# Kernel optimization log

Measured on AMD Instinct MI355X. Metric: run time of the kernel, lower is better.

The kernel has to match this reference:

```python
import jax, jax.numpy as jnp
import numpy as np

IN_DIM = 128
OUT_DIM = 64
ALPHA = 0.2  # LeakyReLU negative slope


def _xavier(key, shape):
    # matches nn.init.xavier_uniform_ with gain=1.414
    fan_in, fan_out = shape
    limit = 1.414 * np.sqrt(6.0 / (fan_in + fan_out))
    return jax.random.uniform(key, shape, jnp.float32, -limit, limit)


def setup_inputs() -> dict:
    key = jax.random.key(0)
    ks = jax.random.split(key, 12)
    N_C, N_P, N_I, E = 200000, 200000, 100000, 1000000
    return {
        "taxPayer_feats": jax.random.normal(ks[0], (N_C, IN_DIM), jnp.float32),
        "person_feats": jax.random.normal(ks[1], (N_P, IN_DIM), jnp.float32),
        "item_feats": jax.random.normal(ks[2], (N_I, IN_DIM), jnp.float32),
        "idx_c0": jax.random.randint(ks[3], (E,), 0, N_C, jnp.int64 if jax.config.jax_enable_x64 else jnp.int32),
        "idx_c1": jax.random.randint(ks[4], (E,), 0, N_C, jnp.int64 if jax.config.jax_enable_x64 else jnp.int32),
        "idx_p": jax.random.randint(ks[5], (E,), 0, N_P, jnp.int64 if jax.config.jax_enable_x64 else jnp.int32),
        "P_company": _xavier(ks[6], (IN_DIM, OUT_DIM)),
        "P_person": _xavier(ks[7], (IN_DIM, OUT_DIM)),
        "P_item": _xavier(ks[8], (IN_DIM, OUT_DIM)),
        "W_PCC": _xavier(ks[9], (OUT_DIM * 3, OUT_DIM)),
    }


def reference(taxPayer_feats, person_feats, item_feats, idx_c0, idx_c1, idx_p,
              P_company, P_person, P_item, W_PCC):
    # InstanceAggLayer.forward, pattern_name='PCC'
    f_taxPayer = taxPayer_feats @ P_company   # [N_C, D]
    f_person = person_feats @ P_person        # [N_P, D]
    f_item = item_feats @ P_item              # computed in original (unused for PCC)
    d = f_taxPayer.shape[1]
    # cat([f_c[i0], f_c[i1], f_p[i2]], dim=1) @ W_PCC  ==  sum of slice matmuls
    # (same math, avoids materializing the [E, 3D] concat)
    pre = (f_taxPayer[idx_c0] @ W_PCC[:d]
           + f_taxPayer[idx_c1] @ W_PCC[d:2 * d]
           + f_person[idx_p] @ W_PCC[2 * d:])
    instance = jnp.where(pre >= 0, pre, ALPHA * pre)  # LeakyReLU
    return instance
```

## Files before the change

kernel.cpp:

```cpp
#include <hip/hip_runtime.h>

#define IN_DIM 128
#define OUT_DIM 64
#define ALPHA 0.2f

typedef __attribute__((ext_vector_type(8))) short short8v;
typedef __attribute__((ext_vector_type(4))) float f32x4;
typedef __attribute__((ext_vector_type(4))) unsigned int u32x4;

__device__ __forceinline__ unsigned short bf16rne(float x) {
    union { float f; unsigned u; } c; c.f = x;
    const unsigned u = c.u;
    return (unsigned short)((u + 0x7fffu + ((u >> 16) & 1u)) >> 16);
}

__global__ __launch_bounds__(256) void compute_M_kernel(
    const float* __restrict__ P_company,
    const float* __restrict__ P_person,
    const float* __restrict__ W_PCC,
    float* __restrict__ M,
    unsigned short* __restrict__ Mt)
{
    const int mb = blockIdx.x >> 4;
    const int chunk = blockIdx.x & 15;
    const float* __restrict__ P = (mb == 2) ? P_person : P_company;
    const float* __restrict__ Wb = W_PCC + mb * OUT_DIM * OUT_DIM;
    float* __restrict__ Mb = M + mb * IN_DIM * OUT_DIM;
    const int base = chunk * 512;
    for (int idx = base + threadIdx.x; idx < base + 512; idx += 256) {
        const int r = idx >> 6;
        const int c = idx & 63;
        float acc = 0.f;
#pragma unroll
        for (int k = 0; k < OUT_DIM; ++k)
            acc = fmaf(P[r * OUT_DIM + k], Wb[k * OUT_DIM + c], acc);
        Mb[idx] = acc;
        Mt[(mb * OUT_DIM + c) * IN_DIM + r] = bf16rne(acc);
    }
}

union F4 { f32x4 v; float f[4]; };

__device__ __forceinline__ void load_A(F4* L, const float* __restrict__ feats,
                                       int nrows, int tile, int fr, int fq) {
    long long ar = (long long)tile * 16 + fr;
    if (ar >= nrows) ar = nrows - 1;
    const float* __restrict__ A = feats + ar * IN_DIM;
#pragma unroll
    for (int k0i = 0; k0i < 4; ++k0i) {
        L[k0i * 2 + 0].v = __builtin_nontemporal_load(
            (const f32x4*)(A + k0i * 32 + fq * 4));
        L[k0i * 2 + 1].v = __builtin_nontemporal_load(
            (const f32x4*)(A + k0i * 32 + 16 + fq * 4));
    }
}

__device__ __forceinline__ void table_body(
    const float* __restrict__ feats, int nrows,
    const unsigned short* __restrict__ Mtb,
    unsigned short* __restrict__ out,
    int tile0, int tstride)
{
    const int lane = threadIdx.x & 63;
    const int fr   = lane & 15;
    const int fq   = lane >> 4;

    union FragU { short8v v; uint2 q[2]; };
    short8v bfrag[4][4];
#pragma unroll
    for (int k0i = 0; k0i < 4; ++k0i)
#pragma unroll
        for (int c0i = 0; c0i < 4; ++c0i) {
            const unsigned short* p =
                Mtb + ((size_t)(c0i * 16 + fr)) * IN_DIM + k0i * 32 + fq * 4;
            FragU f;
            f.q[0] = *(const uint2*)(p);
            f.q[1] = *(const uint2*)(p + 16);
            bfrag[k0i][c0i] = f.v;
        }

    const int ntiles = (nrows + 15) >> 4;
    union AF { short8v v; unsigned short u[8]; };

    int tile = tile0;
    if (tile >= ntiles) return;
    F4 La[8];
    load_A(La, feats, nrows, tile, fr, fq);

    for (; tile < ntiles; tile += tstride) {
        const int next = tile + tstride;
        F4 Lb[8];
        if (next < ntiles) load_A(Lb, feats, nrows, next, fr, fq);

        short8v afrag[4];
#pragma unroll
        for (int k0i = 0; k0i < 4; ++k0i) {
            AF af;
#pragma unroll
            for (int j = 0; j < 4; ++j) {
                af.u[j]     = bf16rne(La[k0i * 2 + 0].f[j]);
                af.u[4 + j] = bf16rne(La[k0i * 2 + 1].f[j]);
            }
            afrag[k0i] = af.v;
        }

        f32x4 acc[4];
#pragma unroll
        for (int c0i = 0; c0i < 4; ++c0i) acc[c0i] = (f32x4){0.f, 0.f, 0.f, 0.f};
#pragma unroll
        for (int k0i = 0; k0i < 4; ++k0i)
#pragma unroll
            for (int c0i = 0; c0i < 4; ++c0i)
                acc[c0i] = __builtin_amdgcn_mfma_f32_16x16x32_bf16(
                    afrag[k0i], bfrag[k0i][c0i], acc[c0i], 0, 0, 0);

        const long long row0 = (long long)tile * 16;
#pragma unroll
        for (int c0i = 0; c0i < 4; ++c0i)
#pragma unroll
            for (int j = 0; j < 4; ++j) {
                const long long rg = row0 + fq * 4 + j;
                if (rg < nrows)
                    out[rg * OUT_DIM + c0i * 16 + fr] = bf16rne(acc[c0i][j]);
            }

#pragma unroll
        for (int i = 0; i < 8; ++i) La[i] = Lb[i];
    }
}

__global__ __launch_bounds__(256) void tables_kernel(
    const float* __restrict__ T, int n_c,
    const float* __restrict__ Pp, int n_p,
    const unsigned short* __restrict__ Mt,
    unsigned short* __restrict__ g0,
    unsigned short* __restrict__ g2,
    int gsplit)
{
    const int w = threadIdx.x >> 6;
    if ((int)blockIdx.x < gsplit) {
        const int table = w & 1;
        const int tile0 = (int)blockIdx.x * 2 + (w >> 1);
        table_body(T, n_c,
                   Mt + (size_t)table * OUT_DIM * IN_DIM,
                   g0 + (size_t)table * n_c * OUT_DIM,
                   tile0, gsplit * 2);
    } else {
        const int bid = (int)blockIdx.x - gsplit;
        const int nb  = (int)gridDim.x - gsplit;
        table_body(Pp, n_p,
                   Mt + (size_t)2 * OUT_DIM * IN_DIM,
                   g2, bid * 4 + w, nb * 4);
    }
}

__global__ __launch_bounds__(256) void gather_kernel(
    const int* __restrict__ i0, const int* __restrict__ i1, const int* __restrict__ i2,
    const unsigned short* __restrict__ g0, const unsigned short* __restrict__ g1,
    const unsigned short* __restrict__ g2,
    float* __restrict__ out, long long E)
{
    const long long t = (long long)blockIdx.x * 256 + threadIdx.x;
    const long long grp = t >> 3;
    const int j = (int)t & 7;
    const long long e0 = grp * 4;
    if (e0 >= E) return;

    long long e[4];
    bool live[4];
#pragma unroll
    for (int k = 0; k < 4; ++k) {
        e[k] = e0 + k;
        live[k] = e[k] < E;
        if (!live[k]) e[k] = E - 1;
    }

    int a0[4], a1[4], a2[4];
#pragma unroll
    for (int k = 0; k < 4; ++k) {
        a0[k] = __builtin_nontemporal_load(i0 + e[k]);
        a1[k] = __builtin_nontemporal_load(i1 + e[k]);
        a2[k] = __builtin_nontemporal_load(i2 + e[k]);
    }

    u32x4 v0[4], v1[4], v2[4];
#pragma unroll
    for (int k = 0; k < 4; ++k) {
        v0[k] = *(const u32x4*)(g0 + (long long)a0[k] * OUT_DIM + j * 8);
        v1[k] = *(const u32x4*)(g1 + (long long)a1[k] * OUT_DIM + j * 8);
        v2[k] = *(const u32x4*)(g2 + (long long)a2[k] * OUT_DIM + j * 8);
    }

#pragma unroll
    for (int k = 0; k < 4; ++k) {
        float s[8];
#pragma unroll
        for (int m = 0; m < 4; ++m) {
            const unsigned u0 = v0[k][m], u1 = v1[k][m], u2 = v2[k][m];
            const float lo = __uint_as_float(u0 << 16)
                           + __uint_as_float(u1 << 16)
                           + __uint_as_float(u2 << 16);
            const float hi = __uint_as_float(u0 & 0xffff0000u)
                           + __uint_as_float(u1 & 0xffff0000u)
                           + __uint_as_float(u2 & 0xffff0000u);
            s[2 * m]     = lo >= 0.f ? lo : ALPHA * lo;
            s[2 * m + 1] = hi >= 0.f ? hi : ALPHA * hi;
        }
        if (live[k]) {
            float* __restrict__ o = out + e[k] * OUT_DIM + j * 8;
            const f32x4 q0 = {s[0], s[1], s[2], s[3]};
            const f32x4 q1 = {s[4], s[5], s[6], s[7]};
            __builtin_nontemporal_store(q0, (f32x4*)(o));
            __builtin_nontemporal_store(q1, (f32x4*)(o + 4));
        }
    }
}

__global__ __launch_bounds__(256) void fused_fallback_kernel(
    const float* __restrict__ T, const float* __restrict__ Pp,
    const int* __restrict__ i0, const int* __restrict__ i1, const int* __restrict__ i2,
    const float* __restrict__ M, float* __restrict__ out, long long E)
{
    const int wave = threadIdx.x >> 6;
    const int lane = threadIdx.x & 63;
    const long long wavesTotal = (long long)gridDim.x * 4;
    const float* __restrict__ M0 = M;
    const float* __restrict__ M1 = M + IN_DIM * OUT_DIM;
    const float* __restrict__ M2 = M + 2 * IN_DIM * OUT_DIM;
    for (long long e = (long long)blockIdx.x * 4 + wave; e < E; e += wavesTotal) {
        const float* __restrict__ x0 = T + (long long)i0[e] * IN_DIM;
        const float* __restrict__ x1 = T + (long long)i1[e] * IN_DIM;
        const float* __restrict__ x2 = Pp + (long long)i2[e] * IN_DIM;
        float acc = 0.f;
#pragma unroll 4
        for (int k = 0; k < IN_DIM; ++k) {
            acc = fmaf(x0[k], M0[k * OUT_DIM + lane], acc);
            acc = fmaf(x1[k], M1[k * OUT_DIM + lane], acc);
            acc = fmaf(x2[k], M2[k * OUT_DIM + lane], acc);
        }
        acc = acc >= 0.f ? acc : ALPHA * acc;
        out[e * OUT_DIM + lane] = acc;
    }
}

extern "C" void kernel_launch(void* const* d_in, const int* in_sizes, int n_in,
                              void* d_out, int out_size, void* d_ws, size_t ws_size,
                              hipStream_t stream) {
    const float* T    = (const float*)d_in[0];
    const float* Pp   = (const float*)d_in[1];
    const int*   i0   = (const int*)d_in[3];
    const int*   i1   = (const int*)d_in[4];
    const int*   i2   = (const int*)d_in[5];
    const float* Pc   = (const float*)d_in[6];
    const float* Pper = (const float*)d_in[7];
    const float* W    = (const float*)d_in[9];
    float* out = (float*)d_out;

    const int n_c = in_sizes[0] / IN_DIM;
    const int n_p = in_sizes[1] / IN_DIM;
    const long long E = in_sizes[3];

    float* M = (float*)d_ws;
    unsigned short* Mt = (unsigned short*)((char*)d_ws + 98304);
    const size_t tblOff = 98304 + 49152;
    const size_t tblBytes = ((size_t)n_c * 2 + (size_t)n_p) * OUT_DIM * sizeof(unsigned short);

    compute_M_kernel<<<48, 256, 0, stream>>>(Pc, Pper, W, M, Mt);

    if (ws_size >= tblOff + tblBytes) {
        unsigned short* g0 = (unsigned short*)((char*)d_ws + tblOff);
        unsigned short* g1 = g0 + (size_t)n_c * OUT_DIM;
        unsigned short* g2 = g1 + (size_t)n_c * OUT_DIM;

        const int GA = 1024;
        const int GB = 512;
        tables_kernel<<<GA + GB, 256, 0, stream>>>(T, n_c, Pp, n_p, Mt, g0, g2, GA);

        const long long groups = (E + 3) / 4;
        const long long threads = groups * 8;
        gather_kernel<<<(int)((threads + 255) / 256), 256, 0, stream>>>(
            i0, i1, i2, g0, g1, g2, out, E);
    } else {
        fused_fallback_kernel<<<16384, 256, 0, stream>>>(T, Pp, i0, i1, i2, M, out, E);
    }
}
```

Baseline: 203.8 us.

## Stage feature rows in LDS as bf16 and use one block per tile

The tables kernel now gives each block a 64-row tile. The block loads that tile cooperatively with coalesced float4 reads, converts it to bf16 once, and stores it in shared memory. For the company table, both projection waves then read the same staged rows, so each feature row is converted once instead of once per table. The old persistent grid-stride loop with register prefetch is replaced by a grid sized to the row count, which removes manual software pipelining in exchange for more blocks and a barrier. The gather kernel also switches from nontemporal to ordinary index loads and output stores.

```diff
diff --git a/kernel.cpp b/kernel.cpp
--- a/kernel.cpp
+++ b/kernel.cpp
@@ -3,6 +3,8 @@
 #define IN_DIM 128
 #define OUT_DIM 64
 #define ALPHA 0.2f
+#define TROWS 64
+#define LROW (IN_DIM + 4)
 
 typedef __attribute__((ext_vector_type(8))) short short8v;
 typedef __attribute__((ext_vector_type(4))) float f32x4;
@@ -39,31 +41,39 @@
     }
 }
 
-union F4 { f32x4 v; float f[4]; };
-
-__device__ __forceinline__ void load_A(F4* L, const float* __restrict__ feats,
-                                       int nrows, int tile, int fr, int fq) {
-    long long ar = (long long)tile * 16 + fr;
-    if (ar >= nrows) ar = nrows - 1;
-    const float* __restrict__ A = feats + ar * IN_DIM;
-#pragma unroll
-    for (int k0i = 0; k0i < 4; ++k0i) {
-        L[k0i * 2 + 0].v = __builtin_nontemporal_load(
-            (const f32x4*)(A + k0i * 32 + fq * 4));
-        L[k0i * 2 + 1].v = __builtin_nontemporal_load(
-            (const f32x4*)(A + k0i * 32 + 16 + fq * 4));
-    }
-}
-
-__device__ __forceinline__ void table_body(
-    const float* __restrict__ feats, int nrows,
-    const unsigned short* __restrict__ Mtb,
-    unsigned short* __restrict__ out,
-    int tile0, int tstride)
-{
+__global__ __launch_bounds__(256) void tables_kernel(
+    const float* __restrict__ T, int n_c,
+    const float* __restrict__ Pp, int n_p,
+    const unsigned short* __restrict__ Mt,
+    unsigned short* __restrict__ g0,
+    unsigned short* __restrict__ g2,
+    int gsplit)
+{
+    __shared__ unsigned short xs[TROWS][LROW];
+    const int w    = threadIdx.x >> 6;
     const int lane = threadIdx.x & 63;
     const int fr   = lane & 15;
     const int fq   = lane >> 4;
+
+    const float* __restrict__ feats;
+    const unsigned short* __restrict__ Mtb;
+    unsigned short* __restrict__ outp;
+    int nrows, t0, tcount;
+    long long row0;
+    if ((int)blockIdx.x < gsplit) {
+        feats = T; nrows = n_c;
+        row0  = (long long)blockIdx.x * TROWS;
+        const int table = w & 1;
+        Mtb  = Mt + (size_t)table * OUT_DIM * IN_DIM;
+        outp = g0 + (size_t)table * n_c * OUT_DIM;
+        t0 = (w >> 1) * 2; tcount = 2;
+    } else {
+        feats = Pp; nrows = n_p;
+        row0  = (long long)((int)blockIdx.x - gsplit) * TROWS;
+        Mtb  = Mt + (size_t)2 * OUT_DIM * IN_DIM;
+        outp = g2;
+        t0 = w; tcount = 1;
+    }
 
     union FragU { short8v v; uint2 q[2]; };
     short8v bfrag[4][4];
@@ -79,28 +89,28 @@
             bfrag[k0i][c0i] = f.v;
         }
 
-    const int ntiles = (nrows + 15) >> 4;
-    union AF { short8v v; unsigned short u[8]; };
-
-    int tile = tile0;
-    if (tile >= ntiles) return;
-    F4 La[8];
-    load_A(La, feats, nrows, tile, fr, fq);
-
-    for (; tile < ntiles; tile += tstride) {
-        const int next = tile + tstride;
-        F4 Lb[8];
-        if (next < ntiles) load_A(Lb, feats, nrows, next, fr, fq);
-
+    for (int i = threadIdx.x; i < TROWS * (IN_DIM / 4); i += 256) {
+        const int r  = i >> 5;
+        const int c4 = i & 31;
+        long long gr = row0 + r;
+        if (gr >= nrows) gr = nrows - 1;
+        const float4 v = *(const float4*)(feats + gr * IN_DIM + c4 * 4);
+        union { unsigned short s[4]; uint2 q; } b;
+        b.s[0] = bf16rne(v.x); b.s[1] = bf16rne(v.y);
+        b.s[2] = bf16rne(v.z); b.s[3] = bf16rne(v.w);
+        *(uint2*)&xs[r][c4 * 4] = b.q;
+    }
+    __syncthreads();
+
+    const bool full = (row0 + TROWS) <= (long long)nrows;
+    for (int ti = 0; ti < tcount; ++ti) {
+        const int t = t0 + ti;
         short8v afrag[4];
 #pragma unroll
         for (int k0i = 0; k0i < 4; ++k0i) {
-            AF af;
-#pragma unroll
-            for (int j = 0; j < 4; ++j) {
-                af.u[j]     = bf16rne(La[k0i * 2 + 0].f[j]);
-                af.u[4 + j] = bf16rne(La[k0i * 2 + 1].f[j]);
-            }
+            FragU af;
+            af.q[0] = *(const uint2*)&xs[t * 16 + fr][k0i * 32 + fq * 4];
+            af.q[1] = *(const uint2*)&xs[t * 16 + fr][k0i * 32 + 16 + fq * 4];
             afrag[k0i] = af.v;
         }
 
@@ -114,43 +124,24 @@
                 acc[c0i] = __builtin_amdgcn_mfma_f32_16x16x32_bf16(
                     afrag[k0i], bfrag[k0i][c0i], acc[c0i], 0, 0, 0);
 
-        const long long row0 = (long long)tile * 16;
-#pragma unroll
-        for (int c0i = 0; c0i < 4; ++c0i)
-#pragma unroll
-            for (int j = 0; j < 4; ++j) {
-                const long long rg = row0 + fq * 4 + j;
-                if (rg < nrows)
-                    out[rg * OUT_DIM + c0i * 16 + fr] = bf16rne(acc[c0i][j]);
-            }
-
-#pragma unroll
-        for (int i = 0; i < 8; ++i) La[i] = Lb[i];
-    }
-}
-
-__global__ __launch_bounds__(256) void tables_kernel(
-    const float* __restrict__ T, int n_c,
-    const float* __restrict__ Pp, int n_p,
-    const unsigned short* __restrict__ Mt,
-    unsigned short* __restrict__ g0,
-    unsigned short* __restrict__ g2,
-    int gsplit)
-{
-    const int w = threadIdx.x >> 6;
-    if ((int)blockIdx.x < gsplit) {
-        const int table = w & 1;
-        const int tile0 = (int)blockIdx.x * 2 + (w >> 1);
-        table_body(T, n_c,
-                   Mt + (size_t)table * OUT_DIM * IN_DIM,
-                   g0 + (size_t)table * n_c * OUT_DIM,
-                   tile0, gsplit * 2);
-    } else {
-        const int bid = (int)blockIdx.x - gsplit;
-        const int nb  = (int)gridDim.x - gsplit;
-        table_body(Pp, n_p,
-                   Mt + (size_t)2 * OUT_DIM * IN_DIM,
-                   g2, bid * 4 + w, nb * 4);
+        const long long rowt = row0 + t * 16;
+        if (full) {
+#pragma unroll
+            for (int c0i = 0; c0i < 4; ++c0i)
+#pragma unroll
+                for (int j = 0; j < 4; ++j)
+                    outp[(rowt + fq * 4 + j) * OUT_DIM + c0i * 16 + fr] =
+                        bf16rne(acc[c0i][j]);
+        } else {
+#pragma unroll
+            for (int c0i = 0; c0i < 4; ++c0i)
+#pragma unroll
+                for (int j = 0; j < 4; ++j) {
+                    const long long rg = rowt + fq * 4 + j;
+                    if (rg < nrows)
+                        outp[rg * OUT_DIM + c0i * 16 + fr] = bf16rne(acc[c0i][j]);
+                }
+        }
     }
 }
 
@@ -178,9 +169,9 @@
     int a0[4], a1[4], a2[4];
 #pragma unroll
     for (int k = 0; k < 4; ++k) {
-        a0[k] = __builtin_nontemporal_load(i0 + e[k]);
-        a1[k] = __builtin_nontemporal_load(i1 + e[k]);
-        a2[k] = __builtin_nontemporal_load(i2 + e[k]);
+        a0[k] = i0[e[k]];
+        a1[k] = i1[e[k]];
+        a2[k] = i2[e[k]];
     }
 
     u32x4 v0[4], v1[4], v2[4];
@@ -208,10 +199,8 @@
         }
         if (live[k]) {
             float* __restrict__ o = out + e[k] * OUT_DIM + j * 8;
-            const f32x4 q0 = {s[0], s[1], s[2], s[3]};
-            const f32x4 q1 = {s[4], s[5], s[6], s[7]};
-            __builtin_nontemporal_store(q0, (f32x4*)(o));
-            __builtin_nontemporal_store(q1, (f32x4*)(o + 4));
+            *(float4*)(o)     = make_float4(s[0], s[1], s[2], s[3]);
+            *(float4*)(o + 4) = make_float4(s[4], s[5], s[6], s[7]);
         }
     }
 }
@@ -272,8 +261,8 @@
         unsigned short* g1 = g0 + (size_t)n_c * OUT_DIM;
         unsigned short* g2 = g1 + (size_t)n_c * OUT_DIM;
 
-        const int GA = 1024;
-        const int GB = 512;
+        const int GA = (n_c + TROWS - 1) / TROWS;
+        const int GB = (n_p + TROWS - 1) / TROWS;
         tables_kernel<<<GA + GB, 256, 0, stream>>>(T, n_c, Pp, n_p, Mt, g0, g2, GA);
 
         const long long groups = (E + 3) / 4;
```

Result: slower. 232.4 us (+14.0%).
